# Kernel optimization log

Measured on AMD Instinct MI355X. Metric: run time of the kernel, lower is better.

## Reference

```python
import jax, jax.numpy as jnp
import numpy as np

ROAD, ZONE, RD, LD, LN = 200000, 128, 128, 32, 2000
NE, NS = 1600000, 1000000


def setup_inputs() -> dict:
    key = jax.random.key(0)
    ks = jax.random.split(key, 10)
    return {
        "length_feature": jax.random.randint(ks[0], (ROAD,), 0, LN, dtype=jnp.int32),
        "node_feature": jnp.arange(ROAD, dtype=jnp.int32),
        "edge_index": jax.random.randint(ks[1], (2, NE), 0, ROAD, dtype=jnp.int32),
        "struct_assign": jax.random.uniform(ks[2], (ROAD, ZONE), dtype=jnp.float32),
        "s_edge": jax.random.randint(ks[3], (2, NS), 0, ROAD, dtype=jnp.int32),
        "node_emb_table": jax.random.normal(ks[4], (ROAD, RD - LD), dtype=jnp.float32) * 0.02,
        "length_emb_table": jax.random.normal(ks[5], (LN, LD), dtype=jnp.float32) * 0.02,
        "gcn_w": jax.random.normal(ks[6], (RD, ZONE), dtype=jnp.float32) / jnp.sqrt(jnp.float32(RD)),
        "gcn_b": jnp.zeros((ZONE,), dtype=jnp.float32),
        "lin_w": jax.random.normal(ks[7], (3 * RD, 100), dtype=jnp.float32) / jnp.sqrt(jnp.float32(3 * RD)),
        "lin_b": jnp.zeros((100,), dtype=jnp.float32),
    }


def reference(length_feature, node_feature, edge_index, struct_assign, s_edge,
              node_emb_table, length_emb_table, gcn_w, gcn_b, lin_w, lin_b):
    n_road = struct_assign.shape[0]
    # embedding lookups -> raw_feat [road, road_dim]
    raw_feat = jnp.concatenate([length_emb_table[length_feature],
                                node_emb_table[node_feature]], axis=1)
    # column normalization: assign / (relu(colsum - 1) + 1)
    sa = struct_assign / (jax.nn.relu(struct_assign.sum(0) - 1.0) + 1.0)
    # struct_emb [zone, road_dim]
    struct_emb = sa.T @ raw_feat
    # special_spmm: (sparse adj with ones at edges) @ sa  == scatter-add of gathered rows
    struct_inter = jax.ops.segment_sum(sa[edge_index[1]], edge_index[0],
                                       num_segments=n_road)  # [road, zone]
    struct_adj = sa.T @ struct_inter  # [zone, zone]
    # GraphConvolution: adj @ x @ W + b, then softmax over dim 0
    fnc_assign = jax.nn.softmax(struct_adj @ (struct_emb @ gcn_w) + gcn_b, axis=0)
    fnc_emb = fnc_assign.T @ struct_emb  # [zone, road_dim]
    N_C = sa @ struct_emb                # [road, road_dim]
    N_F = (sa @ fnc_assign) @ fnc_emb    # [road, road_dim]
    X = jnp.concatenate([raw_feat, N_C, N_F], axis=1) @ lin_w + lin_b  # [road, 100]
    # edge-wise dot product of gathered rows
    pred_edge = jnp.einsum('ij,ij->i', X[s_edge[0]], X[s_edge[1]])
    return pred_edge, X
```

## Files before the change

kernel.cpp:

```cpp
#include <hip/hip_runtime.h>
#include <cstdint>
#include <cstddef>

#define ROADN 200000
#define NEDGE 1600000
#define NSEDGE 1000000
#define NP1 512
#define NP2 1024
#define PSPLIT 16
#define T8PAD 40
#define WXPAD 264

typedef __attribute__((ext_vector_type(8))) short s16x8;
typedef __attribute__((ext_vector_type(4))) float f32x4;

union FragU { int i[4]; s16x8 s; };
union Byte16 { s16x8 v; unsigned char b[16]; };

__device__ inline void cvt_split8(const float v[8], s16x8& hi, s16x8& lo) {
  FragU H, L;
  float lof[8];
#pragma unroll
  for (int p = 0; p < 4; ++p) {
    int h;
    asm("v_cvt_pk_bf16_f32 %0, %1, %2" : "=v"(h) : "v"(v[2 * p]), "v"(v[2 * p + 1]));
    H.i[p] = h;
    float h0 = __builtin_bit_cast(float, (unsigned)h << 16);
    float h1 = __builtin_bit_cast(float, (unsigned)h & 0xFFFF0000u);
    lof[2 * p] = v[2 * p] - h0;
    lof[2 * p + 1] = v[2 * p + 1] - h1;
  }
#pragma unroll
  for (int p = 0; p < 4; ++p) {
    int l;
    asm("v_cvt_pk_bf16_f32 %0, %1, %2" : "=v"(l) : "v"(lof[2 * p]), "v"(lof[2 * p + 1]));
    L.i[p] = l;
  }
  hi = H.s; lo = L.s;
}

__device__ inline ushort cvt1_bf16(float v) {
  float z = 0.f;
  int h;
  asm("v_cvt_pk_bf16_f32 %0, %1, %2" : "=v"(h) : "v"(v), "v"(z));
  return (ushort)(h & 0xFFFF);
}

__global__ __launch_bounds__(256) void k_abf(const float* __restrict__ A,
                                             unsigned char* __restrict__ Abf8,
                                             float* __restrict__ cs) {
  __shared__ float csl[128];
  int t = threadIdx.x;
  if (t < 128) csl[t] = 0.f;
  __syncthreads();
  float ps[8] = {0.f, 0.f, 0.f, 0.f, 0.f, 0.f, 0.f, 0.f};
  const size_t ngroups = (size_t)ROADN * 128 / 8;
  for (size_t g = blockIdx.x * 256ull + threadIdx.x; g < ngroups;
       g += (size_t)gridDim.x * 256ull) {
    const float* p = A + g * 8;
    float4 u0 = *reinterpret_cast<const float4*>(p);
    float4 u1 = *reinterpret_cast<const float4*>(p + 4);
    float v[8] = {u0.x, u0.y, u0.z, u0.w, u1.x, u1.y, u1.z, u1.w};
#pragma unroll
    for (int j = 0; j < 8; ++j) ps[j] += v[j];
    int p0 = __builtin_amdgcn_cvt_pk_fp8_f32(v[0], v[1], 0, false);
    p0 = __builtin_amdgcn_cvt_pk_fp8_f32(v[2], v[3], p0, true);
    int p1 = __builtin_amdgcn_cvt_pk_fp8_f32(v[4], v[5], 0, false);
    p1 = __builtin_amdgcn_cvt_pk_fp8_f32(v[6], v[7], p1, true);
    int2 pk = make_int2(p0, p1);
    *reinterpret_cast<int2*>(Abf8 + g * 8) = pk;
  }
  int cb = (t * 8) & 127;
#pragma unroll
  for (int j = 0; j < 8; ++j)
    atomicAdd(&csl[cb + j], ps[j]);
  __syncthreads();
  if (t < 128) atomicAdd(&cs[t], csl[t]);
}

__global__ __launch_bounds__(256, 4) void k_t2(const unsigned char* __restrict__ Abf8,
                                               const int* __restrict__ ei,
                                               float* __restrict__ PT2) {
  __shared__ unsigned char Td8[2][128 * T8PAD];
  __shared__ unsigned char Ts8[2][128 * T8PAD];
  int t = threadIdx.x;
  int w = t >> 6, l = t & 63;
  int lg = l >> 4, lc = l & 15;
  int half = t >> 7;
  int rp = t & 15;
  int sg = (t >> 4) & 7;
  const int* eibase = ei + (size_t)half * NEDGE;
  const int tiles = NEDGE / 32;
  const int tpb = (tiles + NP2 - 1) / NP2;
  int t0 = blockIdx.x * tpb;
  int t1e = min(t0 + tpb, tiles);

  f32x4 acc[8][2];
#pragma unroll
  for (int m = 0; m < 8; ++m)
#pragma unroll
    for (int n = 0; n < 2; ++n) acc[m][n] = (f32x4){0.f, 0.f, 0.f, 0.f};

  Byte16 v0, v1;
#define T2_LOAD(tt)                                                            \
  {                                                                            \
    int ebase = (tt) * 32;                                                     \
    int2 rr2 = *reinterpret_cast<const int2*>(eibase + ebase + 2 * rp);        \
    v0.v = *reinterpret_cast<const s16x8*>(Abf8 + (size_t)rr2.x * 128 + sg * 16); \
    v1.v = *reinterpret_cast<const s16x8*>(Abf8 + (size_t)rr2.y * 128 + sg * 16); \
  }

  if (t0 < t1e) T2_LOAD(t0);
  int cur = 0;
  for (int tt = t0; tt < t1e; ++tt) {
    unsigned char* buf = half ? Ts8[cur] : Td8[cur];
#pragma unroll
    for (int i = 0; i < 16; ++i) {
      int c = sg * 16 + i;
      *reinterpret_cast<ushort*>(buf + c * T8PAD + 2 * rp) =
          (ushort)v0.b[i] | ((ushort)v1.b[i] << 8);
    }
    if (tt + 1 < t1e) T2_LOAD(tt + 1);
    __syncthreads();
    long bh[2];
#pragma unroll
    for (int n = 0; n < 2; ++n)
      bh[n] = *reinterpret_cast<const long*>(
          &Ts8[cur][(w * 32 + n * 16 + lc) * T8PAD + lg * 8]);
#pragma unroll
    for (int m = 0; m < 8; ++m) {
      long ah = *reinterpret_cast<const long*>(
          &Td8[cur][(m * 16 + lc) * T8PAD + lg * 8]);
#pragma unroll
      for (int n = 0; n < 2; ++n)
        acc[m][n] = __builtin_amdgcn_mfma_f32_16x16x32_fp8_fp8(ah, bh[n], acc[m][n], 0, 0, 0);
    }
    cur ^= 1;
  }
#undef T2_LOAD
  float* out = PT2 + (size_t)blockIdx.x * 16384;
#pragma unroll
  for (int m = 0; m < 8; ++m)
#pragma unroll
    for (int n = 0; n < 2; ++n)
#pragma unroll
      for (int r = 0; r < 4; ++r) {
        int row = m * 16 + lg * 4 + r;
        int col = (2 * w + n) * 16 + lc;
        out[row * 128 + col] = acc[m][n][r];
      }
}

__global__ __launch_bounds__(256) void k_t1(
    const float* __restrict__ A,
    const int* __restrict__ lf, const int* __restrict__ nf,
    const float* __restrict__ lemb, const float* __restrict__ nemb,
    float* __restrict__ PT1) {
  int t = threadIdx.x;
  int w = t >> 6, l = t & 63;
  int lg = l >> 4, lc = l & 15;
  const int tiles = ROADN / 32;
  const int tpb = (tiles + NP1 - 1) / NP1;
  int t0 = blockIdx.x * tpb;
  int t1e = min(t0 + tpb, tiles);

  f32x4 acc[8][2];
#pragma unroll
  for (int m = 0; m < 8; ++m)
#pragma unroll
    for (int n = 0; n < 2; ++n) acc[m][n] = (f32x4){0.f, 0.f, 0.f, 0.f};

  const int* idxp = (w == 0) ? lf : nf;

  for (int tt = t0; tt < t1e; ++tt) {
    int roff = tt * 32 + lg * 8;
    int4 i0 = *reinterpret_cast<const int4*>(idxp + roff);
    int4 i1 = *reinterpret_cast<const int4*>(idxp + roff + 4);
    int iv[8] = {i0.x, i0.y, i0.z, i0.w, i1.x, i1.y, i1.z, i1.w};
    const float* ap[8];
    const float* bp[8];
#pragma unroll
    for (int e = 0; e < 8; ++e) {
      ap[e] = A + (size_t)(roff + e) * 128 + lc;
      bp[e] = (w == 0) ? (lemb + (size_t)iv[e] * 32 + lc)
                       : (nemb + (size_t)iv[e] * 96 + (w * 32 - 32) + lc);
    }
    s16x8 bhi[2], blo[2];
#pragma unroll
    for (int n = 0; n < 2; ++n) {
      float bv[8];
#pragma unroll
      for (int e = 0; e < 8; ++e) bv[e] = bp[e][n * 16];
      cvt_split8(bv, bhi[n], blo[n]);
    }
#pragma unroll
    for (int m = 0; m < 8; ++m) {
      float av[8];
#pragma unroll
      for (int e = 0; e < 8; ++e) av[e] = ap[e][m * 16];
      s16x8 ahi, alo;
      cvt_split8(av, ahi, alo);
#pragma unroll
      for (int n = 0; n < 2; ++n) {
        acc[m][n] = __builtin_amdgcn_mfma_f32_16x16x32_bf16(ahi, bhi[n], acc[m][n], 0, 0, 0);
        acc[m][n] = __builtin_amdgcn_mfma_f32_16x16x32_bf16(ahi, blo[n], acc[m][n], 0, 0, 0);
        acc[m][n] = __builtin_amdgcn_mfma_f32_16x16x32_bf16(alo, bhi[n], acc[m][n], 0, 0, 0);
      }
    }
  }
  float* out = PT1 + (size_t)blockIdx.x * 16384;
#pragma unroll
  for (int m = 0; m < 8; ++m)
#pragma unroll
    for (int n = 0; n < 2; ++n)
#pragma unroll
      for (int r = 0; r < 4; ++r) {
        int row = m * 16 + lg * 4 + r;
        int col = (2 * w + n) * 16 + lc;
        out[row * 128 + col] = acc[m][n][r];
      }
}

__global__ __launch_bounds__(256) void k_reduce(const float* __restrict__ PT1,
                                                const float* __restrict__ PT2,
                                                float* __restrict__ T1,
                                                float* __restrict__ T2) {
  int b = blockIdx.x;
  int which = b & 1;
  int echunk = (b >> 1) & 63;
  int pchunk = b >> 7;
  const float* P = which ? PT2 : PT1;
  int np = which ? NP2 : NP1;
  int ppc = np / PSPLIT;
  int e = echunk * 256 + threadIdx.x;
  const float* base = P + (size_t)pchunk * ppc * 16384 + e;
  float s = 0.f;
  for (int p = 0; p < ppc; ++p)
    s += base[(size_t)p * 16384];
  atomicAdd((which ? T2 : T1) + e, s);
}

#define ACC4(crow, lv, r4) \
  crow[0] += (lv) * (r4).x; crow[1] += (lv) * (r4).y; \
  crow[2] += (lv) * (r4).z; crow[3] += (lv) * (r4).w;

__global__ __launch_bounds__(1024) void k_small(
    const float* __restrict__ T1, const float* __restrict__ T2,
    const float* __restrict__ cs, const float* __restrict__ gcn_w,
    const float* __restrict__ gcn_b, const float* __restrict__ lin_w,
    float* __restrict__ Gg, float* __restrict__ FEg,
    float* __restrict__ W12) {
  __shared__ float SE[128 * 128];
  __shared__ float FA[128 * 128];
  __shared__ float sc[128];
  int t = threadIdx.x;
  int ty = t >> 5, tx = t & 31;
  if (t < 128) {
    float s = cs[t] - 1.f;
    sc[t] = 1.f / (fmaxf(s, 0.f) + 1.f);
  }
  __syncthreads();
  for (int idx = t; idx < 16384; idx += 1024)
    SE[idx] = sc[idx >> 7] * T1[idx];
  __syncthreads();
  {
    float c0[4] = {0,0,0,0}, c1[4] = {0,0,0,0}, c2[4] = {0,0,0,0}, c3[4] = {0,0,0,0};
    for (int m = 0; m < 128; ++m) {
      float4 r = *reinterpret_cast<const float4*>(gcn_w + m * 128 + tx * 4);
      float l0 = SE[(ty * 4 + 0) * 128 + m];
      float l1 = SE[(ty * 4 + 1) * 128 + m];
      float l2 = SE[(ty * 4 + 2) * 128 + m];
      float l3 = SE[(ty * 4 + 3) * 128 + m];
      ACC4(c0, l0, r); ACC4(c1, l1, r); ACC4(c2, l2, r); ACC4(c3, l3, r);
    }
    float* cr[4] = {c0, c1, c2, c3};
#pragma unroll
    for (int a = 0; a < 4; ++a) {
      int i = ty * 4 + a;
      float4 o = make_float4(sc[i]*cr[a][0], sc[i]*cr[a][1], sc[i]*cr[a][2], sc[i]*cr[a][3]);
      *reinterpret_cast<float4*>(Gg + i * 128 + tx * 4) = o;
    }
  }
  __syncthreads();
  {
    float c0[4] = {0,0,0,0}, c1[4] = {0,0,0,0}, c2[4] = {0,0,0,0}, c3[4] = {0,0,0,0};
    for (int m = 0; m < 128; ++m) {
      float4 r = *reinterpret_cast<const float4*>(Gg + m * 128 + tx * 4);
      float l0 = T2[(ty * 4 + 0) * 128 + m];
      float l1 = T2[(ty * 4 + 1) * 128 + m];
      float l2 = T2[(ty * 4 + 2) * 128 + m];
      float l3 = T2[(ty * 4 + 3) * 128 + m];
      ACC4(c0, l0, r); ACC4(c1, l1, r); ACC4(c2, l2, r); ACC4(c3, l3, r);
    }
    float4 b4 = *reinterpret_cast<const float4*>(gcn_b + tx * 4);
    float* cr[4] = {c0, c1, c2, c3};
#pragma unroll
    for (int a = 0; a < 4; ++a) {
      int i = ty * 4 + a;
      FA[i * 128 + tx * 4 + 0] = sc[i] * cr[a][0] + b4.x;
      FA[i * 128 + tx * 4 + 1] = sc[i] * cr[a][1] + b4.y;
      FA[i * 128 + tx * 4 + 2] = sc[i] * cr[a][2] + b4.z;
      FA[i * 128 + tx * 4 + 3] = sc[i] * cr[a][3] + b4.w;
    }
  }
  __syncthreads();
  if (t < 128) {
    int j = t;
    float mx = -3.4e38f;
    for (int i = 0; i < 128; ++i) mx = fmaxf(mx, FA[i * 128 + j]);
    float sum = 0.f;
    for (int i = 0; i < 128; ++i) {
      float e = expf(FA[i * 128 + j] - mx);
      FA[i * 128 + j] = e;
      sum += e;
    }
    float inv = 1.f / sum;
    for (int i = 0; i < 128; ++i) FA[i * 128 + j] *= inv;
  }
  __syncthreads();
  {
    float c0[4] = {0,0,0,0}, c1[4] = {0,0,0,0}, c2[4] = {0,0,0,0}, c3[4] = {0,0,0,0};
    for (int m = 0; m < 128; ++m) {
      float4 r = *reinterpret_cast<const float4*>(&SE[m * 128 + tx * 4]);
      float l0 = FA[m * 128 + ty * 4 + 0];
      float l1 = FA[m * 128 + ty * 4 + 1];
      float l2 = FA[m * 128 + ty * 4 + 2];
      float l3 = FA[m * 128 + ty * 4 + 3];
      ACC4(c0, l0, r); ACC4(c1, l1, r); ACC4(c2, l2, r); ACC4(c3, l3, r);
    }
    float* cr[4] = {c0, c1, c2, c3};
#pragma unroll
    for (int a = 0; a < 4; ++a) {
      float4 o = make_float4(cr[a][0], cr[a][1], cr[a][2], cr[a][3]);
      *reinterpret_cast<float4*>(FEg + (ty * 4 + a) * 128 + tx * 4) = o;
    }
  }
  __syncthreads();
  {
    float c0[4] = {0,0,0,0}, c1[4] = {0,0,0,0}, c2[4] = {0,0,0,0}, c3[4] = {0,0,0,0};
    for (int m = 0; m < 128; ++m) {
      float4 r = *reinterpret_cast<const float4*>(FEg + m * 128 + tx * 4);
      float l0 = FA[(ty * 4 + 0) * 128 + m];
      float l1 = FA[(ty * 4 + 1) * 128 + m];
      float l2 = FA[(ty * 4 + 2) * 128 + m];
      float l3 = FA[(ty * 4 + 3) * 128 + m];
      ACC4(c0, l0, r); ACC4(c1, l1, r); ACC4(c2, l2, r); ACC4(c3, l3, r);
    }
    __syncthreads();
    float* cr[4] = {c0, c1, c2, c3};
#pragma unroll
    for (int a = 0; a < 4; ++a) {
      int i = ty * 4 + a;
      FA[i * 128 + tx * 4 + 0] = cr[a][0];
      FA[i * 128 + tx * 4 + 1] = cr[a][1];
      FA[i * 128 + tx * 4 + 2] = cr[a][2];
      FA[i * 128 + tx * 4 + 3] = cr[a][3];
    }
  }
  __syncthreads();
  if (tx < 25) {
    float c0[4] = {0,0,0,0}, c1[4] = {0,0,0,0}, c2[4] = {0,0,0,0}, c3[4] = {0,0,0,0};
    for (int j = 0; j < 128; ++j) {
      float4 r1 = *reinterpret_cast<const float4*>(lin_w + (128 + j) * 100 + tx * 4);
      float4 r2 = *reinterpret_cast<const float4*>(lin_w + (256 + j) * 100 + tx * 4);
      float s0 = SE[(ty * 4 + 0) * 128 + j], f0 = FA[(ty * 4 + 0) * 128 + j];
      float s1 = SE[(ty * 4 + 1) * 128 + j], f1 = FA[(ty * 4 + 1) * 128 + j];
      float s2 = SE[(ty * 4 + 2) * 128 + j], f2 = FA[(ty * 4 + 2) * 128 + j];
      float s3 = SE[(ty * 4 + 3) * 128 + j], f3 = FA[(ty * 4 + 3) * 128 + j];
      ACC4(c0, s0, r1); ACC4(c0, f0, r2);
      ACC4(c1, s1, r1); ACC4(c1, f1, r2);
      ACC4(c2, s2, r1); ACC4(c2, f2, r2);
      ACC4(c3, s3, r1); ACC4(c3, f3, r2);
    }
    float* cr[4] = {c0, c1, c2, c3};
#pragma unroll
    for (int a = 0; a < 4; ++a) {
      int k = ty * 4 + a;
#pragma unroll
      for (int b = 0; b < 4; ++b)
        W12[k * 100 + tx * 4 + b] = sc[k] * cr[a][b];
    }
  }
}

__global__ __launch_bounds__(256) void k_wt(const float* __restrict__ lin_w,
                                            const float* __restrict__ W12,
                                            ushort* __restrict__ WThi,
                                            ushort* __restrict__ WTlo) {
  int idx = blockIdx.x * 256 + threadIdx.x;
  if (idx >= 112 * 256) return;
  int col = idx >> 8;
  int k = idx & 255;
  float v = 0.f;
  if (col < 100)
    v = (k < 128) ? lin_w[k * 100 + col] : W12[(k - 128) * 100 + col];
  float z = 0.f;
  int h;
  asm("v_cvt_pk_bf16_f32 %0, %1, %2" : "=v"(h) : "v"(v), "v"(z));
  ushort hu = (ushort)(h & 0xFFFF);
  float hf = __builtin_bit_cast(float, (unsigned)hu << 16);
  float lof = v - hf;
  int lw2;
  asm("v_cvt_pk_bf16_f32 %0, %1, %2" : "=v"(lw2) : "v"(lof), "v"(z));
  WThi[idx] = hu;
  WTlo[idx] = (ushort)(lw2 & 0xFFFF);
}

__global__ __launch_bounds__(1024, 4) void k_x(
    const float* __restrict__ A, const int* __restrict__ lf,
    const int* __restrict__ nf, const float* __restrict__ lemb,
    const float* __restrict__ nemb, const float* __restrict__ lin_b,
    const ushort* __restrict__ WThi, const ushort* __restrict__ WTlo,
    float* __restrict__ X, ushort* __restrict__ Xbf) {
  __shared__ ushort Whl[2][112 * WXPAD];
  int t = threadIdx.x;
  for (int i = t; i < 112 * 256; i += 1024) {
    int col = i >> 8;
    int k = i & 255;
    int d = col * WXPAD + k;
    Whl[0][d] = WThi[i];
    Whl[1][d] = WTlo[i];
  }
  __syncthreads();

  int wid = t >> 6, l = t & 63;
  int lg = l >> 4, lc = l & 15;
  int rb0 = blockIdx.x * 512 + wid * 32;
  if (rb0 >= ROADN) return;

  float bias[7];
#pragma unroll
  for (int n = 0; n < 7; ++n) {
    int c = n * 16 + lc;
    bias[n] = (c < 100) ? lin_b[c] : 0.f;
  }

  f32x4 acc[2][7];
#pragma unroll
  for (int m = 0; m < 2; ++m)
#pragma unroll
    for (int n = 0; n < 7; ++n) acc[m][n] = (f32x4){0.f, 0.f, 0.f, 0.f};

  int rr[2], lfv[2], nfv[2];
#pragma unroll
  for (int m = 0; m < 2; ++m) {
    int r = rb0 + m * 16 + lc;
    rr[m] = min(r, ROADN - 1);
    lfv[m] = lf[rr[m]];
    nfv[m] = nf[rr[m]];
  }

#pragma unroll
  for (int ks = 0; ks < 8; ++ks) {
    int kk = ks * 32;
    s16x8 ahi[2], alo[2];
#pragma unroll
    for (int m = 0; m < 2; ++m) {
      const float* p;
      if (ks == 0)
        p = lemb + (size_t)lfv[m] * 32 + lg * 8;
      else if (ks < 4)
        p = nemb + (size_t)nfv[m] * 96 + (kk - 32) + lg * 8;
      else
        p = A + (size_t)rr[m] * 128 + (kk - 128) + lg * 8;
      float4 u0 = *reinterpret_cast<const float4*>(p);
      float4 u1 = *reinterpret_cast<const float4*>(p + 4);
      float av[8] = {u0.x, u0.y, u0.z, u0.w, u1.x, u1.y, u1.z, u1.w};
      cvt_split8(av, ahi[m], alo[m]);
    }
#pragma unroll
    for (int n = 0; n < 7; ++n) {
      int off = (n * 16 + lc) * WXPAD + kk + lg * 8;
      s16x8 bh = *reinterpret_cast<const s16x8*>(&Whl[0][off]);
      s16x8 bl = *reinterpret_cast<const s16x8*>(&Whl[1][off]);
#pragma unroll
      for (int m = 0; m < 2; ++m) {
        acc[m][n] = __builtin_amdgcn_mfma_f32_16x16x32_bf16(ahi[m], bh, acc[m][n], 0, 0, 0);
        acc[m][n] = __builtin_amdgcn_mfma_f32_16x16x32_bf16(ahi[m], bl, acc[m][n], 0, 0, 0);
        acc[m][n] = __builtin_amdgcn_mfma_f32_16x16x32_bf16(alo[m], bh, acc[m][n], 0, 0, 0);
      }
    }
  }
#pragma unroll
  for (int m = 0; m < 2; ++m)
#pragma unroll
    for (int n = 0; n < 7; ++n) {
      int col = n * 16 + lc;
#pragma unroll
      for (int r4 = 0; r4 < 4; ++r4) {
        int row = rb0 + m * 16 + lg * 4 + r4;
        if (row < ROADN) {
          float v = acc[m][n][r4] + bias[n];
          if (col < 100) {
            X[(size_t)row * 100 + col] = v;
            Xbf[(size_t)row * 128 + col] = cvt1_bf16(v);
          } else {
            Xbf[(size_t)row * 128 + col] = 0;
          }
        }
      }
    }
}

__global__ __launch_bounds__(256) void k_pred(const ushort* __restrict__ Xbf,
                                              const int* __restrict__ se,
                                              float* __restrict__ out) {
  unsigned tid = blockIdx.x * 256u + threadIdx.x;
  unsigned e = tid >> 5, lane = tid & 31;
  int ra = se[e];
  int rb = se[NSEDGE + e];
  float acc = 0.f;
  if (lane < 28) {
    const ushort* xa = Xbf + (size_t)ra * 128 + lane * 4;
    const ushort* xb = Xbf + (size_t)rb * 128 + lane * 4;
    ushort4 a = *reinterpret_cast<const ushort4*>(xa);
    ushort4 b = *reinterpret_cast<const ushort4*>(xb);
    float ax = __builtin_bit_cast(float, (unsigned)a.x << 16);
    float ay = __builtin_bit_cast(float, (unsigned)a.y << 16);
    float az = __builtin_bit_cast(float, (unsigned)a.z << 16);
    float aw = __builtin_bit_cast(float, (unsigned)a.w << 16);
    float bx = __builtin_bit_cast(float, (unsigned)b.x << 16);
    float by = __builtin_bit_cast(float, (unsigned)b.y << 16);
    float bz = __builtin_bit_cast(float, (unsigned)b.z << 16);
    float bw = __builtin_bit_cast(float, (unsigned)b.w << 16);
    acc = ax * bx + ay * by + az * bz + aw * bw;
  }
#pragma unroll
  for (int off = 16; off > 0; off >>= 1)
    acc += __shfl_xor(acc, off, 32);
  if (lane == 0) out[e] = acc;
}

extern "C" void kernel_launch(void* const* d_in, const int* in_sizes, int n_in,
                              void* d_out, int out_size, void* d_ws, size_t ws_size,
                              hipStream_t stream) {
  const int*   lf   = (const int*)d_in[0];
  const int*   nf   = (const int*)d_in[1];
  const int*   ei   = (const int*)d_in[2];
  const float* A    = (const float*)d_in[3];
  const int*   se   = (const int*)d_in[4];
  const float* nemb = (const float*)d_in[5];
  const float* lemb = (const float*)d_in[6];
  const float* gw   = (const float*)d_in[7];
  const float* gb   = (const float*)d_in[8];
  const float* lw   = (const float*)d_in[9];
  const float* lb   = (const float*)d_in[10];

  float* ws  = (float*)d_ws;
  float* PT1 = ws;
  float* PT2 = PT1 + (size_t)NP1 * 16384;
  float* T1  = PT2 + (size_t)NP2 * 16384;
  float* T2  = T1 + 16384;
  float* cs  = T2 + 16384;
  float* Gg  = cs + 128;
  float* FEg = Gg + 16384;
  float* W12 = FEg + 16384;
  ushort* WThi = (ushort*)(W12 + 12800);
  ushort* WTlo = WThi + 112 * 256;

  float* pred = (float*)d_out;
  float* X    = pred + NSEDGE;
  unsigned char* Abf8 = (unsigned char*)X;
  ushort* Xbf = (ushort*)PT1;

  hipMemsetAsync(T1, 0, (size_t)(16384 * 2 + 128) * sizeof(float), stream);

  k_abf<<<2048, 256, 0, stream>>>(A, Abf8, cs);
  k_t1<<<NP1, 256, 0, stream>>>(A, lf, nf, lemb, nemb, PT1);
  k_t2<<<NP2, 256, 0, stream>>>(Abf8, ei, PT2);
  k_reduce<<<2 * 64 * PSPLIT, 256, 0, stream>>>(PT1, PT2, T1, T2);
  k_small<<<1, 1024, 0, stream>>>(T1, T2, cs, gw, gb, lw, Gg, FEg, W12);
  k_wt<<<112, 256, 0, stream>>>(lw, W12, WThi, WTlo);
  k_x<<<(ROADN + 511) / 512, 1024, 0, stream>>>(A, lf, nf, lemb, nemb, lb, WThi, WTlo, X, Xbf);
  k_pred<<<(NSEDGE * 32) / 256, 256, 0, stream>>>(Xbf, se, pred);
}
```

Baseline: 528.6 us.

## Split single-block small-matrix kernel into multiple grid-parallel kernels

```diff
diff --git a/kernel.cpp b/kernel.cpp
--- a/kernel.cpp
+++ b/kernel.cpp
@@ -44,6 +44,11 @@
   int h;
   asm("v_cvt_pk_bf16_f32 %0, %1, %2" : "=v"(h) : "v"(v), "v"(z));
   return (ushort)(h & 0xFFFF);
+}
+
+__device__ inline float sc_of(const float* cs, int i) {
+  float s = cs[i] - 1.f;
+  return 1.f / (fmaxf(s, 0.f) + 1.f);
 }
 
 __global__ __launch_bounds__(256) void k_abf(const float* __restrict__ A,
@@ -240,147 +245,84 @@
   atomicAdd((which ? T2 : T1) + e, s);
 }
 
-#define ACC4(crow, lv, r4) \
-  crow[0] += (lv) * (r4).x; crow[1] += (lv) * (r4).y; \
-  crow[2] += (lv) * (r4).z; crow[3] += (lv) * (r4).w;
-
-__global__ __launch_bounds__(1024) void k_small(
-    const float* __restrict__ T1, const float* __restrict__ T2,
-    const float* __restrict__ cs, const float* __restrict__ gcn_w,
-    const float* __restrict__ gcn_b, const float* __restrict__ lin_w,
-    float* __restrict__ Gg, float* __restrict__ FEg,
-    float* __restrict__ W12) {
-  __shared__ float SE[128 * 128];
-  __shared__ float FA[128 * 128];
-  __shared__ float sc[128];
-  int t = threadIdx.x;
-  int ty = t >> 5, tx = t & 31;
-  if (t < 128) {
-    float s = cs[t] - 1.f;
-    sc[t] = 1.f / (fmaxf(s, 0.f) + 1.f);
-  }
-  __syncthreads();
-  for (int idx = t; idx < 16384; idx += 1024)
-    SE[idx] = sc[idx >> 7] * T1[idx];
-  __syncthreads();
-  {
-    float c0[4] = {0,0,0,0}, c1[4] = {0,0,0,0}, c2[4] = {0,0,0,0}, c3[4] = {0,0,0,0};
-    for (int m = 0; m < 128; ++m) {
-      float4 r = *reinterpret_cast<const float4*>(gcn_w + m * 128 + tx * 4);
-      float l0 = SE[(ty * 4 + 0) * 128 + m];
-      float l1 = SE[(ty * 4 + 1) * 128 + m];
-      float l2 = SE[(ty * 4 + 2) * 128 + m];
-      float l3 = SE[(ty * 4 + 3) * 128 + m];
-      ACC4(c0, l0, r); ACC4(c1, l1, r); ACC4(c2, l2, r); ACC4(c3, l3, r);
-    }
-    float* cr[4] = {c0, c1, c2, c3};
-#pragma unroll
-    for (int a = 0; a < 4; ++a) {
-      int i = ty * 4 + a;
-      float4 o = make_float4(sc[i]*cr[a][0], sc[i]*cr[a][1], sc[i]*cr[a][2], sc[i]*cr[a][3]);
-      *reinterpret_cast<float4*>(Gg + i * 128 + tx * 4) = o;
-    }
-  }
-  __syncthreads();
-  {
-    float c0[4] = {0,0,0,0}, c1[4] = {0,0,0,0}, c2[4] = {0,0,0,0}, c3[4] = {0,0,0,0};
-    for (int m = 0; m < 128; ++m) {
-      float4 r = *reinterpret_cast<const float4*>(Gg + m * 128 + tx * 4);
-      float l0 = T2[(ty * 4 + 0) * 128 + m];
-      float l1 = T2[(ty * 4 + 1) * 128 + m];
-      float l2 = T2[(ty * 4 + 2) * 128 + m];
-      float l3 = T2[(ty * 4 + 3) * 128 + m];
-      ACC4(c0, l0, r); ACC4(c1, l1, r); ACC4(c2, l2, r); ACC4(c3, l3, r);
-    }
-    float4 b4 = *reinterpret_cast<const float4*>(gcn_b + tx * 4);
-    float* cr[4] = {c0, c1, c2, c3};
-#pragma unroll
-    for (int a = 0; a < 4; ++a) {
-      int i = ty * 4 + a;
-      FA[i * 128 + tx * 4 + 0] = sc[i] * cr[a][0] + b4.x;
-      FA[i * 128 + tx * 4 + 1] = sc[i] * cr[a][1] + b4.y;
-      FA[i * 128 + tx * 4 + 2] = sc[i] * cr[a][2] + b4.z;
-      FA[i * 128 + tx * 4 + 3] = sc[i] * cr[a][3] + b4.w;
-    }
-  }
-  __syncthreads();
-  if (t < 128) {
-    int j = t;
-    float mx = -3.4e38f;
-    for (int i = 0; i < 128; ++i) mx = fmaxf(mx, FA[i * 128 + j]);
-    float sum = 0.f;
-    for (int i = 0; i < 128; ++i) {
-      float e = expf(FA[i * 128 + j] - mx);
-      FA[i * 128 + j] = e;
-      sum += e;
-    }
-    float inv = 1.f / sum;
-    for (int i = 0; i < 128; ++i) FA[i * 128 + j] *= inv;
-  }
-  __syncthreads();
-  {
-    float c0[4] = {0,0,0,0}, c1[4] = {0,0,0,0}, c2[4] = {0,0,0,0}, c3[4] = {0,0,0,0};
-    for (int m = 0; m < 128; ++m) {
-      float4 r = *reinterpret_cast<const float4*>(&SE[m * 128 + tx * 4]);
-      float l0 = FA[m * 128 + ty * 4 + 0];
-      float l1 = FA[m * 128 + ty * 4 + 1];
-      float l2 = FA[m * 128 + ty * 4 + 2];
-      float l3 = FA[m * 128 + ty * 4 + 3];
-      ACC4(c0, l0, r); ACC4(c1, l1, r); ACC4(c2, l2, r); ACC4(c3, l3, r);
-    }
-    float* cr[4] = {c0, c1, c2, c3};
-#pragma unroll
-    for (int a = 0; a < 4; ++a) {
-      float4 o = make_float4(cr[a][0], cr[a][1], cr[a][2], cr[a][3]);
-      *reinterpret_cast<float4*>(FEg + (ty * 4 + a) * 128 + tx * 4) = o;
-    }
-  }
-  __syncthreads();
-  {
-    float c0[4] = {0,0,0,0}, c1[4] = {0,0,0,0}, c2[4] = {0,0,0,0}, c3[4] = {0,0,0,0};
-    for (int m = 0; m < 128; ++m) {
-      float4 r = *reinterpret_cast<const float4*>(FEg + m * 128 + tx * 4);
-      float l0 = FA[(ty * 4 + 0) * 128 + m];
-      float l1 = FA[(ty * 4 + 1) * 128 + m];
-      float l2 = FA[(ty * 4 + 2) * 128 + m];
-      float l3 = FA[(ty * 4 + 3) * 128 + m];
-      ACC4(c0, l0, r); ACC4(c1, l1, r); ACC4(c2, l2, r); ACC4(c3, l3, r);
-    }
-    __syncthreads();
-    float* cr[4] = {c0, c1, c2, c3};
-#pragma unroll
-    for (int a = 0; a < 4; ++a) {
-      int i = ty * 4 + a;
-      FA[i * 128 + tx * 4 + 0] = cr[a][0];
-      FA[i * 128 + tx * 4 + 1] = cr[a][1];
-      FA[i * 128 + tx * 4 + 2] = cr[a][2];
-      FA[i * 128 + tx * 4 + 3] = cr[a][3];
-    }
-  }
-  __syncthreads();
-  if (tx < 25) {
-    float c0[4] = {0,0,0,0}, c1[4] = {0,0,0,0}, c2[4] = {0,0,0,0}, c3[4] = {0,0,0,0};
-    for (int j = 0; j < 128; ++j) {
-      float4 r1 = *reinterpret_cast<const float4*>(lin_w + (128 + j) * 100 + tx * 4);
-      float4 r2 = *reinterpret_cast<const float4*>(lin_w + (256 + j) * 100 + tx * 4);
-      float s0 = SE[(ty * 4 + 0) * 128 + j], f0 = FA[(ty * 4 + 0) * 128 + j];
-      float s1 = SE[(ty * 4 + 1) * 128 + j], f1 = FA[(ty * 4 + 1) * 128 + j];
-      float s2 = SE[(ty * 4 + 2) * 128 + j], f2 = FA[(ty * 4 + 2) * 128 + j];
-      float s3 = SE[(ty * 4 + 3) * 128 + j], f3 = FA[(ty * 4 + 3) * 128 + j];
-      ACC4(c0, s0, r1); ACC4(c0, f0, r2);
-      ACC4(c1, s1, r1); ACC4(c1, f1, r2);
-      ACC4(c2, s2, r1); ACC4(c2, f2, r2);
-      ACC4(c3, s3, r1); ACC4(c3, f3, r2);
-    }
-    float* cr[4] = {c0, c1, c2, c3};
-#pragma unroll
-    for (int a = 0; a < 4; ++a) {
-      int k = ty * 4 + a;
-#pragma unroll
-      for (int b = 0; b < 4; ++b)
-        W12[k * 100 + tx * 4 + b] = sc[k] * cr[a][b];
-    }
-  }
+__global__ __launch_bounds__(256) void k_se(const float* __restrict__ T1,
+                                            const float* __restrict__ cs,
+                                            float* __restrict__ SE) {
+  int idx = blockIdx.x * 256 + threadIdx.x;
+  if (idx >= 16384) return;
+  SE[idx] = sc_of(cs, idx >> 7) * T1[idx];
+}
+
+__global__ __launch_bounds__(128) void k_mm1(const float* __restrict__ SE,
+                                             const float* __restrict__ gw,
+                                             const float* __restrict__ cs,
+                                             float* __restrict__ Gg) {
+  int b = blockIdx.x, j = threadIdx.x;
+  const float* Lr = SE + b * 128;
+  float acc = 0.f;
+  for (int k = 0; k < 128; ++k)
+    acc += Lr[k] * gw[k * 128 + j];
+  Gg[b * 128 + j] = sc_of(cs, b) * acc;
+}
+
+__global__ __launch_bounds__(128) void k_mm2(const float* __restrict__ T2,
+                                             const float* __restrict__ Gg,
+                                             const float* __restrict__ cs,
+                                             const float* __restrict__ gb,
+                                             float* __restrict__ FA) {
+  int b = blockIdx.x, j = threadIdx.x;
+  const float* Lr = T2 + b * 128;
+  float acc = 0.f;
+  for (int k = 0; k < 128; ++k)
+    acc += Lr[k] * Gg[k * 128 + j];
+  FA[b * 128 + j] = sc_of(cs, b) * acc + gb[j];
+}
+
+__global__ __launch_bounds__(128) void k_soft(float* __restrict__ FA) {
+  int j = threadIdx.x;
+  float mx = -3.4e38f;
+  for (int i = 0; i < 128; ++i) mx = fmaxf(mx, FA[i * 128 + j]);
+  float sum = 0.f;
+  for (int i = 0; i < 128; ++i) sum += expf(FA[i * 128 + j] - mx);
+  float inv = 1.f / sum;
+  for (int i = 0; i < 128; ++i)
+    FA[i * 128 + j] = expf(FA[i * 128 + j] - mx) * inv;
+}
+
+__global__ __launch_bounds__(128) void k_mm3(const float* __restrict__ FA,
+                                             const float* __restrict__ SE,
+                                             float* __restrict__ FEg) {
+  int i = blockIdx.x, j = threadIdx.x;
+  float acc = 0.f;
+  for (int k = 0; k < 128; ++k)
+    acc += FA[k * 128 + i] * SE[k * 128 + j];
+  FEg[i * 128 + j] = acc;
+}
+
+__global__ __launch_bounds__(128) void k_mm4(const float* __restrict__ FA,
+                                             const float* __restrict__ FEg,
+                                             float* __restrict__ FF) {
+  int b = blockIdx.x, j = threadIdx.x;
+  const float* Lr = FA + b * 128;
+  float acc = 0.f;
+  for (int k = 0; k < 128; ++k)
+    acc += Lr[k] * FEg[k * 128 + j];
+  FF[b * 128 + j] = acc;
+}
+
+__global__ __launch_bounds__(128) void k_w12(const float* __restrict__ SE,
+                                             const float* __restrict__ FF,
+                                             const float* __restrict__ lin_w,
+                                             const float* __restrict__ cs,
+                                             float* __restrict__ W12) {
+  int k = blockIdx.x, c = threadIdx.x;
+  if (c >= 100) return;
+  const float* Sr = SE + k * 128;
+  const float* Fr = FF + k * 128;
+  float acc = 0.f;
+  for (int j = 0; j < 128; ++j)
+    acc += Sr[j] * lin_w[(128 + j) * 100 + c] + Fr[j] * lin_w[(256 + j) * 100 + c];
+  W12[k * 100 + c] = sc_of(cs, k) * acc;
 }
 
 __global__ __launch_bounds__(256) void k_wt(const float* __restrict__ lin_w,
@@ -557,6 +499,9 @@
   float* W12 = FEg + 16384;
   ushort* WThi = (ushort*)(W12 + 12800);
   ushort* WTlo = WThi + 112 * 256;
+  float* SEb = (float*)(WTlo + 112 * 256);
+  float* FAb = SEb + 16384;
+  float* FFb = FAb + 16384;
 
   float* pred = (float*)d_out;
   float* X    = pred + NSEDGE;
@@ -569,7 +514,13 @@
   k_t1<<<NP1, 256, 0, stream>>>(A, lf, nf, lemb, nemb, PT1);
   k_t2<<<NP2, 256, 0, stream>>>(Abf8, ei, PT2);
   k_reduce<<<2 * 64 * PSPLIT, 256, 0, stream>>>(PT1, PT2, T1, T2);
-  k_small<<<1, 1024, 0, stream>>>(T1, T2, cs, gw, gb, lw, Gg, FEg, W12);
+  k_se<<<64, 256, 0, stream>>>(T1, cs, SEb);
+  k_mm1<<<128, 128, 0, stream>>>(SEb, gw, cs, Gg);
+  k_mm2<<<128, 128, 0, stream>>>(T2, Gg, cs, gb, FAb);
+  k_soft<<<1, 128, 0, stream>>>(FAb);
+  k_mm3<<<128, 128, 0, stream>>>(FAb, SEb, FEg);
+  k_mm4<<<128, 128, 0, stream>>>(FAb, FEg, FFb);
+  k_w12<<<128, 128, 0, stream>>>(SEb, FFb, lw, cs, W12);
   k_wt<<<112, 256, 0, stream>>>(lw, W12, WThi, WTlo);
   k_x<<<(ROADN + 511) / 512, 1024, 0, stream>>>(A, lf, nf, lemb, nemb, lb, WThi, WTlo, X, Xbf);
   k_pred<<<(NSEDGE * 32) / 256, 256, 0, stream>>>(Xbf, se, pred);
```

Result: faster. 480.8 us (-9.0%).
